# Kernel optimization log

Hardware: AMD Instinct MI355X
Metric: run time of the kernel (lower is better)

Reference implementation:

```python
import jax, jax.numpy as jnp
import numpy as np


def setup_inputs() -> dict:
    key = jax.random.key(0)
    k1, k2, k3, k4 = jax.random.split(key, 4)
    B, S, H = 1, 2048, 3072
    E, I = 4, 8192  # num_experts, intermediate_size
    x = jax.random.normal(k1, (B, S, H), dtype=jnp.float32)
    gate_w = jax.random.normal(k2, (E, H), dtype=jnp.float32) * 0.02
    w_gate_up = jax.random.normal(k3, (E, 2 * I, H), dtype=jnp.float32) * 0.02
    w_down = jax.random.normal(k4, (E, H, I), dtype=jnp.float32) * 0.02
    return {"x": x, "gate_w": gate_w, "w_gate_up": w_gate_up, "w_down": w_down, "top_k": 2}


def reference(x, gate_w, w_gate_up, w_down, top_k):
    # x: [B, S, H]; gate_w: [E, H]; w_gate_up: [E, 2I, H]; w_down: [E, H, I]
    B, S, H = x.shape
    E = gate_w.shape[0]
    # Gating: softmax over experts, then top-k values/indices
    logits = jnp.einsum('bsh,eh->bse', x, gate_w)
    probs = jax.nn.softmax(logits, axis=-1)
    gate_values, gate_indices = jax.lax.top_k(probs, top_k)  # [B, S, k]
    # Dense all-expert SwiGLU MLP (as in the original module)
    xf = x.reshape(-1, H)                                     # [N, H]
    up_states = jnp.einsum('nh,eih->nei', xf, w_gate_up)      # [N, E, 2I]
    gate, up = jnp.split(up_states, 2, axis=-1)               # [N, E, I] each
    hidden = up * jax.nn.silu(gate)                           # SwiGLU
    expert_out = jnp.einsum('nei,ehi->neh', hidden, w_down)   # [N, E, H]
    expert_out = expert_out.reshape(B, S, E, H)
    # Gather selected experts and combine with gate values
    sel = jnp.take_along_axis(expert_out, gate_indices[..., None], axis=2)  # [B, S, k, H]
    moe_output = jnp.sum(sel * gate_values[..., None], axis=2)              # [B, S, H]
    return moe_output
```

## Files before the change

kernel.cpp:

```cpp
#include <hip/hip_runtime.h>

#define S 2048
#define Hd 3072
#define NE 4
#define Id 8192
#define BK 64
#define RMAX 5120

typedef __attribute__((ext_vector_type(8))) short short8;
typedef __attribute__((ext_vector_type(4))) float f32x4;

__device__ __forceinline__ unsigned short f2bf(float f) {
    unsigned u = __builtin_bit_cast(unsigned, f);
    u += 0x7FFFu + ((u >> 16) & 1u);
    return (unsigned short)(u >> 16);
}

__device__ __forceinline__ void gload_lds16(const void* g, void* l) {
    __builtin_amdgcn_global_load_lds(
        (const __attribute__((address_space(1))) unsigned int*)g,
        (__attribute__((address_space(3))) unsigned int*)l,
        16, 0, 0);
}

#define BAR_SB()  { __builtin_amdgcn_s_barrier(); __builtin_amdgcn_sched_barrier(0); }
#define LGKM0_SB() { asm volatile("s_waitcnt lgkmcnt(0)" ::: "memory"); __builtin_amdgcn_sched_barrier(0); }
#define VM6_SB()  { asm volatile("s_waitcnt vmcnt(6)" ::: "memory"); __builtin_amdgcn_sched_barrier(0); }

__global__ void gate_topk_kernel(const float* __restrict__ x,
                                 const float* __restrict__ gw,
                                 int* __restrict__ tok_e,
                                 float* __restrict__ tok_v) {
    const int t = blockIdx.x;
    const int lane = threadIdx.x & 63;
    const int wave = threadIdx.x >> 6;
    __shared__ float logits[NE];
    const float* xp = x + (size_t)t * Hd;
    const float* wp = gw + (size_t)wave * Hd;
    float s = 0.f;
    for (int h = lane; h < Hd; h += 64) s += xp[h] * wp[h];
#pragma unroll
    for (int o = 32; o > 0; o >>= 1) s += __shfl_xor(s, o);
    if (lane == 0) logits[wave] = s;
    __syncthreads();
    if (threadIdx.x == 0) {
        float m = logits[0];
#pragma unroll
        for (int e = 1; e < NE; e++) m = fmaxf(m, logits[e]);
        float p[NE]; float sum = 0.f;
#pragma unroll
        for (int e = 0; e < NE; e++) { p[e] = expf(logits[e] - m); sum += p[e]; }
        float inv = 1.f / sum;
#pragma unroll
        for (int e = 0; e < NE; e++) p[e] *= inv;
        int e0 = 0; float v0 = p[0];
#pragma unroll
        for (int e = 1; e < NE; e++) if (p[e] > v0) { e0 = e; v0 = p[e]; }
        int e1 = -1; float v1 = -1.f;
#pragma unroll
        for (int e = 0; e < NE; e++) if (e != e0 && p[e] > v1) { e1 = e; v1 = p[e]; }
        tok_e[t * 2] = e0; tok_e[t * 2 + 1] = e1;
        tok_v[t * 2] = v0; tok_v[t * 2 + 1] = v1;
    }
}

__global__ void route_kernel(const int* __restrict__ tok_e, const float* __restrict__ tok_v,
                             int* __restrict__ row_token, float* __restrict__ row_gate,
                             int* __restrict__ offsets) {
    __shared__ int cnt[NE], cur[NE], offs[NE + 1];
    const int tid = threadIdx.x;
    if (tid < NE) { cnt[tid] = 0; cur[tid] = 0; }
    __syncthreads();
    for (int i = tid; i < S * 2; i += 256) atomicAdd(&cnt[tok_e[i]], 1);
    __syncthreads();
    if (tid == 0) {
        int o = 0;
        for (int e = 0; e < NE; e++) { offs[e] = o; o += (cnt[e] + 255) / 256 * 256; }
        offs[NE] = o;
        for (int e = 0; e <= NE; e++) offsets[e] = offs[e];
    }
    __syncthreads();
    for (int r = tid; r < RMAX; r += 256) { row_token[r] = 0; row_gate[r] = 0.f; }
    __syncthreads();
    for (int i = tid; i < S * 2; i += 256) {
        int e = tok_e[i];
        int pos = atomicAdd(&cur[e], 1);
        int r = offs[e] + pos;
        row_token[r] = i >> 1;
        row_gate[r] = tok_v[i];
    }
}

__global__ void cvt_bf16_kernel(const float* __restrict__ src,
                                unsigned short* __restrict__ dst, size_t n8) {
    size_t stride = (size_t)gridDim.x * blockDim.x;
    for (size_t i = (size_t)blockIdx.x * blockDim.x + threadIdx.x; i < n8; i += stride) {
        size_t b = i * 8;
        f32x4 a = *(const f32x4*)(src + b);
        f32x4 c = *(const f32x4*)(src + b + 4);
        union { unsigned short u[8]; short8 v; } o;
#pragma unroll
        for (int j = 0; j < 4; j++) { o.u[j] = f2bf(a[j]); o.u[4 + j] = f2bf(c[j]); }
        *(short8*)(dst + b) = o.v;
    }
}


#define ST_A0(buf, k) { gload_lds16(aP[0] + (k), &Ald[buf][raD[0]][0]); gload_lds16(aP[1] + (k), &Ald[buf][raD[1]][0]); }
#define ST_A1(buf, k) { gload_lds16(aP[2] + (k), &Ald[buf][raD[2]][0]); gload_lds16(aP[3] + (k), &Ald[buf][raD[3]][0]); }
#define ST_B0(buf, k) { gload_lds16(bP[0] + (k), &Bld[buf][rbD[0]][0]); gload_lds16(bP[1] + (k), &Bld[buf][rbD[1]][0]); }
#define ST_B1(buf, k) { gload_lds16(bP[2] + (k), &Bld[buf][rbD[2]][0]); gload_lds16(bP[3] + (k), &Bld[buf][rbD[3]][0]); }

#define READ_AFL(b) _Pragma("unroll") for (int mi = 0; mi < 4; mi++) _Pragma("unroll") for (int kk = 0; kk < 2; kk++) { \
    int row = wm * 128 + mi * 16 + c16; int slot = ((kk << 2) + c4) ^ l7; \
    afL[mi][kk] = *(const short8*)&Ald[b][row][slot * 8]; }
#define READ_AFH(b) _Pragma("unroll") for (int mi = 0; mi < 4; mi++) _Pragma("unroll") for (int kk = 0; kk < 2; kk++) { \
    int row = wm * 128 + 64 + mi * 16 + c16; int slot = ((kk << 2) + c4) ^ l7; \
    afH[mi][kk] = *(const short8*)&Ald[b][row][slot * 8]; }
#define READ_BFL(b) _Pragma("unroll") for (int n = 0; n < 2; n++) _Pragma("unroll") for (int kk = 0; kk < 2; kk++) { \
    int row = wn * 64 + n * 16 + c16; int slot = ((kk << 2) + c4) ^ l7; \
    bfL[n][kk] = *(const short8*)&Bld[b][row][slot * 8]; }
#define READ_BFH(b) _Pragma("unroll") for (int n = 0; n < 2; n++) _Pragma("unroll") for (int kk = 0; kk < 2; kk++) { \
    int row = wn * 64 + 32 + n * 16 + c16; int slot = ((kk << 2) + c4) ^ l7; \
    bfH[n][kk] = *(const short8*)&Bld[b][row][slot * 8]; }

#define MFMA_Q(AF, BF, MO, NO) _Pragma("unroll") for (int mi = 0; mi < 4; mi++) \
    _Pragma("unroll") for (int n = 0; n < 2; n++) _Pragma("unroll") for (int kk = 0; kk < 2; kk++) \
        acc[mi + MO][n + NO] = __builtin_amdgcn_mfma_f32_16x16x32_bf16(AF[mi][kk], BF[n][kk], acc[mi + MO][n + NO], 0, 0, 0);

#define KTILE_BODY(bR, bW, kN, kNN) { \
    short8 afL[4][2], afH[4][2], bfL[2][2], bfH[2][2]; \
    READ_AFL(bR); READ_BFL(bR); \
    ST_B1(bW, kN); \
    BAR_SB(); LGKM0_SB(); \
    __builtin_amdgcn_s_setprio(1); MFMA_Q(afL, bfL, 0, 0); __builtin_amdgcn_s_setprio(0); \
    BAR_SB(); \
    READ_AFH(bR); \
    ST_A0(bR, kNN); \
    BAR_SB(); LGKM0_SB(); \
    __builtin_amdgcn_s_setprio(1); MFMA_Q(afH, bfL, 4, 0); __builtin_amdgcn_s_setprio(0); \
    BAR_SB(); \
    READ_BFH(bR); \
    ST_B0(bR, kNN); \
    BAR_SB(); LGKM0_SB(); \
    __builtin_amdgcn_s_setprio(1); MFMA_Q(afL, bfH, 0, 2); __builtin_amdgcn_s_setprio(0); \
    BAR_SB(); \
    ST_A1(bR, kNN); \
    BAR_SB(); \
    __builtin_amdgcn_s_setprio(1); MFMA_Q(afH, bfH, 4, 2); __builtin_amdgcn_s_setprio(0); \
    VM6_SB(); BAR_SB(); }

__global__ __launch_bounds__(512, 2)
void gemm1_8p_kernel(const unsigned short* __restrict__ xb,
                     const unsigned short* __restrict__ wgu_b,
                     const int* __restrict__ row_token,
                     const int* __restrict__ offsets,
                     unsigned short* __restrict__ hidden) {
    __shared__ unsigned short Ald[2][256][BK];
    __shared__ unsigned short Bld[2][256][BK];

    const int rt = blockIdx.x, ct = blockIdx.y;
    const int rbase = rt * 256;
    if (rbase >= offsets[4]) return;
    int e = 3;
    if (rbase < offsets[1]) e = 0;
    else if (rbase < offsets[2]) e = 1;
    else if (rbase < offsets[3]) e = 2;

    const int tid = threadIdx.x;
    const int l = tid & 63;
    const int w = tid >> 6;
    const int wm = w >> 2, wn = w & 3;
    const int lr = l >> 3;
    const int g8 = ((l & 7) ^ lr) << 3;
    const int c16 = l & 15, c4 = l >> 4, l7 = l & 7;

    const unsigned short* aP[4]; int raD[4];
    const unsigned short* bP[4]; int rbD[4];
#pragma unroll
    for (int j = 0; j < 4; j++) {
        int r0 = w * 8 + (j & 1) * 128 + (j >> 1) * 64;
        raD[j] = r0;
        int tok = row_token[rbase + r0 + lr];
        aP[j] = xb + (size_t)tok * Hd + g8;
        int rb0 = (w & 3) * 8 + (w >> 2) * 64 + (j & 1) * 128 + (j >> 1) * 32;
        rbD[j] = rb0;
        int brow = rb0 + lr;
        int f = brow >> 4;
        size_t wr = (size_t)e * (2 * Id) + (size_t)(f & 1) * Id
                  + (size_t)ct * 128 + ((f >> 1) << 4) + (brow & 15);
        bP[j] = wgu_b + wr * Hd + g8;
    }

    f32x4 acc[8][4];
#pragma unroll
    for (int mi = 0; mi < 8; mi++)
#pragma unroll
        for (int n = 0; n < 4; n++) acc[mi][n] = (f32x4)0.f;

    ST_A0(0, 0); ST_B0(0, 0); ST_A1(0, 0); ST_B1(0, 0);
    ST_A0(1, BK); ST_B0(1, BK); ST_A1(1, BK);
    VM6_SB(); BAR_SB();

    const int nt = Hd / BK;
    for (int t = 0; t < nt; ++t) {
        const int bR = t & 1, bW = bR ^ 1;
        const int kN  = (t + 1 < nt ? t + 1 : nt - 1) * BK;
        const int kNN = (t + 2 < nt ? t + 2 : nt - 1) * BK;
        KTILE_BODY(bR, bW, kN, kNN);
    }
    asm volatile("s_waitcnt vmcnt(0)" ::: "memory");

#pragma unroll
    for (int mi = 0; mi < 8; mi++)
#pragma unroll
        for (int np = 0; np < 2; np++) {
            int col = ct * 128 + (wn * 2 + np) * 16 + c16;
#pragma unroll
            for (int q = 0; q < 4; q++) {
                int row = rbase + wm * 128 + mi * 16 + c4 * 4 + q;
                float gv = acc[mi][2 * np][q], uv = acc[mi][2 * np + 1][q];
                float h = uv * gv / (1.f + expf(-gv));
                hidden[(size_t)row * Id + col] = f2bf(h);
            }
        }
}

__global__ __launch_bounds__(512, 2)
void gemm2_8p_kernel(const unsigned short* __restrict__ hidden,
                     const unsigned short* __restrict__ wd_b,
                     const int* __restrict__ row_token,
                     const float* __restrict__ row_gate,
                     const int* __restrict__ offsets,
                     float* __restrict__ out) {
    __shared__ unsigned short Ald[2][256][BK];
    __shared__ unsigned short Bld[2][256][BK];

    const int rt = blockIdx.x, ct = blockIdx.y;
    const int rbase = rt * 256;
    if (rbase >= offsets[4]) return;
    int e = 3;
    if (rbase < offsets[1]) e = 0;
    else if (rbase < offsets[2]) e = 1;
    else if (rbase < offsets[3]) e = 2;

    const int tid = threadIdx.x;
    const int l = tid & 63;
    const int w = tid >> 6;
    const int wm = w >> 2, wn = w & 3;
    const int lr = l >> 3;
    const int g8 = ((l & 7) ^ lr) << 3;
    const int c16 = l & 15, c4 = l >> 4, l7 = l & 7;

    const unsigned short* aP[4]; int raD[4];
    const unsigned short* bP[4]; int rbD[4];
#pragma unroll
    for (int j = 0; j < 4; j++) {
        int r0 = w * 8 + (j & 1) * 128 + (j >> 1) * 64;
        raD[j] = r0;
        aP[j] = hidden + (size_t)(rbase + r0 + lr) * Id + g8;
        int rb0 = (w & 3) * 8 + (w >> 2) * 64 + (j & 1) * 128 + (j >> 1) * 32;
        rbD[j] = rb0;
        size_t wr = (size_t)e * Hd + (size_t)ct * 256 + rb0 + lr;
        bP[j] = wd_b + wr * Id + g8;
    }

    f32x4 acc[8][4];
#pragma unroll
    for (int mi = 0; mi < 8; mi++)
#pragma unroll
        for (int n = 0; n < 4; n++) acc[mi][n] = (f32x4)0.f;

    ST_A0(0, 0); ST_B0(0, 0); ST_A1(0, 0); ST_B1(0, 0);
    ST_A0(1, BK); ST_B0(1, BK); ST_A1(1, BK);
    VM6_SB(); BAR_SB();

    const int nt = Id / BK;
    for (int t = 0; t < nt; ++t) {
        const int bR = t & 1, bW = bR ^ 1;
        const int kN  = (t + 1 < nt ? t + 1 : nt - 1) * BK;
        const int kNN = (t + 2 < nt ? t + 2 : nt - 1) * BK;
        KTILE_BODY(bR, bW, kN, kNN);
    }
    asm volatile("s_waitcnt vmcnt(0)" ::: "memory");

#pragma unroll
    for (int mi = 0; mi < 8; mi++)
#pragma unroll
        for (int n = 0; n < 4; n++) {
            int col = ct * 256 + wn * 64 + n * 16 + c16;
#pragma unroll
            for (int q = 0; q < 4; q++) {
                int r = rbase + wm * 128 + mi * 16 + c4 * 4 + q;
                int tok = row_token[r];
                float gv = row_gate[r];
                if (gv != 0.f)
                    atomicAdd(&out[(size_t)tok * Hd + col], gv * acc[mi][n][q]);
            }
        }
}


__global__ __launch_bounds__(256, 2)
void gemm1_f32_kernel(const unsigned short* __restrict__ xb,
                      const float* __restrict__ wgu,
                      const int* __restrict__ row_token,
                      const int* __restrict__ offsets,
                      unsigned short* __restrict__ hidden) {
    __shared__ unsigned short As[128][BK];
    __shared__ unsigned short Bg[128][BK];
    __shared__ unsigned short Bu[128][BK];

    const int rt = blockIdx.x, ct = blockIdx.y;
    const int rbase = rt * 128;
    if (rbase >= offsets[4]) return;
    int e = 3;
    if (rbase < offsets[1]) e = 0;
    else if (rbase < offsets[2]) e = 1;
    else if (rbase < offsets[3]) e = 2;

    const int tid = threadIdx.x;
    const int lane = tid & 63;
    const int wave = tid >> 6;
    const int wm = wave >> 1, wn = wave & 1;

    const unsigned short* asrc[4];
#pragma unroll
    for (int i2 = 0; i2 < 4; i2++) {
        int sgi = i2 * 4 + wave;
        int row = sgi * 8 + (lane >> 3);
        int g = (lane & 7) ^ (row & 7);
        int tok = row_token[rbase + row];
        asrc[i2] = xb + (size_t)tok * Hd + g * 8;
    }
    const int col = tid >> 1;
    const int half = tid & 1;
    const size_t grow = (size_t)e * (2 * Id) + (size_t)ct * 128 + col;
    const float* bsrc_g = wgu + grow * Hd + half * 32;
    const float* bsrc_u = wgu + (grow + (size_t)Id) * Hd + half * 32;
    const int csw = col & 7;

    f32x4 accg[4][4], accu[4][4];
#pragma unroll
    for (int m = 0; m < 4; m++)
#pragma unroll
        for (int n = 0; n < 4; n++) { accg[m][n] = (f32x4)0.f; accu[m][n] = (f32x4)0.f; }

    for (int k0 = 0; k0 < Hd; k0 += BK) {
        __syncthreads();
#pragma unroll
        for (int i2 = 0; i2 < 4; i2++) {
            int sgi = i2 * 4 + wave;
            gload_lds16(asrc[i2] + k0, &As[sgi * 8][0]);
        }
        {
            const float* pg = bsrc_g + k0;
            const float* pu = bsrc_u + k0;
            f32x4 vg[8], vu[8];
#pragma unroll
            for (int j = 0; j < 8; j++) vg[j] = *(const f32x4*)(pg + j * 4);
#pragma unroll
            for (int j = 0; j < 8; j++) vu[j] = *(const f32x4*)(pu + j * 4);
#pragma unroll
            for (int j = 0; j < 4; j++) {
                union { unsigned short u[8]; short8 v8; } wg_, wu_;
#pragma unroll
                for (int q = 0; q < 4; q++) {
                    wg_.u[q] = f2bf(vg[2 * j][q]); wg_.u[4 + q] = f2bf(vg[2 * j + 1][q]);
                    wu_.u[q] = f2bf(vu[2 * j][q]); wu_.u[4 + q] = f2bf(vu[2 * j + 1][q]);
                }
                int gs = (half * 4 + j) ^ csw;
                *(short8*)&Bg[col][gs * 8] = wg_.v8;
                *(short8*)&Bu[col][gs * 8] = wu_.v8;
            }
        }
        __syncthreads();
#pragma unroll
        for (int kk = 0; kk < 2; kk++) {
            short8 af[4], bgf[4], buf_[4];
#pragma unroll
            for (int m = 0; m < 4; m++) {
                int r = wm * 64 + m * 16 + (lane & 15);
                int slot = (kk * 4 + (lane >> 4)) ^ (r & 7);
                af[m] = *(const short8*)&As[r][slot * 8];
            }
#pragma unroll
            for (int n = 0; n < 4; n++) {
                int c = wn * 64 + n * 16 + (lane & 15);
                int slot = (kk * 4 + (lane >> 4)) ^ (c & 7);
                bgf[n] = *(const short8*)&Bg[c][slot * 8];
                buf_[n] = *(const short8*)&Bu[c][slot * 8];
            }
#pragma unroll
            for (int m = 0; m < 4; m++)
#pragma unroll
                for (int n = 0; n < 4; n++) {
                    accg[m][n] = __builtin_amdgcn_mfma_f32_16x16x32_bf16(af[m], bgf[n], accg[m][n], 0, 0, 0);
                    accu[m][n] = __builtin_amdgcn_mfma_f32_16x16x32_bf16(af[m], buf_[n], accu[m][n], 0, 0, 0);
                }
        }
    }
#pragma unroll
    for (int m = 0; m < 4; m++) {
#pragma unroll
        for (int n = 0; n < 4; n++) {
            int c = ct * 128 + wn * 64 + n * 16 + (lane & 15);
#pragma unroll
            for (int q = 0; q < 4; q++) {
                int r = rbase + wm * 64 + m * 16 + (lane >> 4) * 4 + q;
                float g = accg[m][n][q], u = accu[m][n][q];
                float hval = u * g / (1.f + expf(-g));
                hidden[(size_t)r * Id + c] = f2bf(hval);
            }
        }
    }
}

__global__ __launch_bounds__(256, 2)
void gemm2_f32_kernel(const unsigned short* __restrict__ hidden,
                      const float* __restrict__ wd,
                      const int* __restrict__ row_token,
                      const float* __restrict__ row_gate,
                      const int* __restrict__ offsets,
                      float* __restrict__ out) {
    __shared__ unsigned short As[128][BK];
    __shared__ unsigned short Bs[128][BK];

    const int rt = blockIdx.x, ct = blockIdx.y;
    const int rbase = rt * 128;
    if (rbase >= offsets[4]) return;
    int e = 3;
    if (rbase < offsets[1]) e = 0;
    else if (rbase < offsets[2]) e = 1;
    else if (rbase < offsets[3]) e = 2;

    const int tid = threadIdx.x;
    const int lane = tid & 63;
    const int wave = tid >> 6;
    const int wm = wave >> 1, wn = wave & 1;

    const unsigned short* asrc[4];
#pragma unroll
    for (int i2 = 0; i2 < 4; i2++) {
        int sgi = i2 * 4 + wave;
        int row = sgi * 8 + (lane >> 3);
        int g = (lane & 7) ^ (row & 7);
        asrc[i2] = hidden + (size_t)(rbase + row) * Id + g * 8;
    }
    const int col = tid >> 1;
    const int half = tid & 1;
    const float* bsrc = wd + ((size_t)e * Hd + (size_t)ct * 128 + col) * Id + half * 32;
    const int csw = col & 7;

    f32x4 acc[4][4];
#pragma unroll
    for (int m = 0; m < 4; m++)
#pragma unroll
        for (int n = 0; n < 4; n++) acc[m][n] = (f32x4)0.f;

    for (int k0 = 0; k0 < Id; k0 += BK) {
        __syncthreads();
#pragma unroll
        for (int i2 = 0; i2 < 4; i2++) {
            int sgi = i2 * 4 + wave;
            gload_lds16(asrc[i2] + k0, &As[sgi * 8][0]);
        }
        {
            const float* pb = bsrc + k0;
            f32x4 vb[8];
#pragma unroll
            for (int j = 0; j < 8; j++) vb[j] = *(const f32x4*)(pb + j * 4);
#pragma unroll
            for (int j = 0; j < 4; j++) {
                union { unsigned short u[8]; short8 v8; } wb_;
#pragma unroll
                for (int q = 0; q < 4; q++) {
                    wb_.u[q] = f2bf(vb[2 * j][q]); wb_.u[4 + q] = f2bf(vb[2 * j + 1][q]);
                }
                int gs = (half * 4 + j) ^ csw;
                *(short8*)&Bs[col][gs * 8] = wb_.v8;
            }
        }
        __syncthreads();
#pragma unroll
        for (int kk = 0; kk < 2; kk++) {
            short8 af[4], bf[4];
#pragma unroll
            for (int m = 0; m < 4; m++) {
                int r = wm * 64 + m * 16 + (lane & 15);
                int slot = (kk * 4 + (lane >> 4)) ^ (r & 7);
                af[m] = *(const short8*)&As[r][slot * 8];
            }
#pragma unroll
            for (int n = 0; n < 4; n++) {
                int c = wn * 64 + n * 16 + (lane & 15);
                int slot = (kk * 4 + (lane >> 4)) ^ (c & 7);
                bf[n] = *(const short8*)&Bs[c][slot * 8];
            }
#pragma unroll
            for (int m = 0; m < 4; m++)
#pragma unroll
                for (int n = 0; n < 4; n++)
                    acc[m][n] = __builtin_amdgcn_mfma_f32_16x16x32_bf16(af[m], bf[n], acc[m][n], 0, 0, 0);
        }
    }
#pragma unroll
    for (int m = 0; m < 4; m++) {
#pragma unroll
        for (int n = 0; n < 4; n++) {
            int c = ct * 128 + wn * 64 + n * 16 + (lane & 15);
#pragma unroll
            for (int q = 0; q < 4; q++) {
                int r = rbase + wm * 64 + m * 16 + (lane >> 4) * 4 + q;
                int tok = row_token[r];
                float gv = row_gate[r];
                if (gv != 0.f)
                    atomicAdd(&out[(size_t)tok * Hd + c], gv * acc[m][n][q]);
            }
        }
    }
}

extern "C" void kernel_launch(void* const* d_in, const int* in_sizes, int n_in,
                              void* d_out, int out_size, void* d_ws, size_t ws_size,
                              hipStream_t stream) {
    const float* x   = (const float*)d_in[0];
    const float* gw  = (const float*)d_in[1];
    const float* wgu = (const float*)d_in[2];
    const float* wd  = (const float*)d_in[3];
    float* out = (float*)d_out;

    const size_t n_wgu = (size_t)NE * 2 * Id * Hd;
    const size_t n_wd  = (size_t)NE * Hd * Id;

    char* ws = (char*)d_ws;
    size_t o = 0;
    auto alloc = [&](size_t bytes) { void* p = ws + o; o = (o + bytes + 255) & ~(size_t)255; return p; };
    unsigned short* xb      = (unsigned short*)alloc((size_t)S * Hd * 2);
    unsigned short* hidden  = (unsigned short*)alloc((size_t)RMAX * Id * 2);
    int*   row_token = (int*)alloc(RMAX * 4);
    float* row_gate  = (float*)alloc(RMAX * 4);
    int*   offsets   = (int*)alloc(8 * 4);
    int*   tok_e     = (int*)alloc(S * 2 * 4);
    float* tok_v     = (float*)alloc(S * 2 * 4);
    unsigned short* wgu_b = (unsigned short*)alloc(n_wgu * 2);
    unsigned short* wd_b  = (unsigned short*)alloc(n_wd * 2);
    const bool big = (ws_size >= o);

    hipMemsetAsync(d_out, 0, (size_t)S * Hd * 4, stream);
    gate_topk_kernel<<<S, 256, 0, stream>>>(x, gw, tok_e, tok_v);
    route_kernel<<<1, 256, 0, stream>>>(tok_e, tok_v, row_token, row_gate, offsets);
    cvt_bf16_kernel<<<1024, 256, 0, stream>>>(x, xb, (size_t)S * Hd / 8);

    if (big) {
        cvt_bf16_kernel<<<2048, 256, 0, stream>>>(wgu, wgu_b, n_wgu / 8);
        cvt_bf16_kernel<<<2048, 256, 0, stream>>>(wd, wd_b, n_wd / 8);
        gemm1_8p_kernel<<<dim3(RMAX / 256, Id / 128), 512, 0, stream>>>(
            xb, wgu_b, row_token, offsets, hidden);
        gemm2_8p_kernel<<<dim3(RMAX / 256, Hd / 256), 512, 0, stream>>>(
            hidden, wd_b, row_token, row_gate, offsets, out);
    } else {
        gemm1_f32_kernel<<<dim3(RMAX / 128, Id / 128), 256, 0, stream>>>(
            xb, wgu, row_token, offsets, hidden);
        gemm2_f32_kernel<<<dim3(RMAX / 128, Hd / 128), 256, 0, stream>>>(
            hidden, wd, row_token, row_gate, offsets, out);
    }
}
```

Before: 1.238 ms.

## Remap GEMM blocks per XCD, shrink gemm2 N-tile, widen bf16 conversion

Both GEMMs now launch a 1D grid whose block index is remapped so that each XCD owns a contiguous range of column tiles. This is meant to improve L2 reuse of the weight tiles. gemm2 halves its N tile to 128 columns with fewer B loads and accumulators, which gives more blocks to fill the CUs at the cost of more re-reads of the A (hidden) tile. The conversion kernel now processes 16 floats per thread with more blocks. The sched_barrier after s_barrier is dropped, which gives the compiler more freedom to schedule but may disturb the hand-tuned ordering.

```diff
diff --git a/kernel.cpp b/kernel.cpp
--- a/kernel.cpp
+++ b/kernel.cpp
@@ -23,9 +23,10 @@
         16, 0, 0);
 }
 
-#define BAR_SB()  { __builtin_amdgcn_s_barrier(); __builtin_amdgcn_sched_barrier(0); }
+#define BAR() __builtin_amdgcn_s_barrier();
 #define LGKM0_SB() { asm volatile("s_waitcnt lgkmcnt(0)" ::: "memory"); __builtin_amdgcn_sched_barrier(0); }
 #define VM6_SB()  { asm volatile("s_waitcnt vmcnt(6)" ::: "memory"); __builtin_amdgcn_sched_barrier(0); }
+#define VM4_SB()  { asm volatile("s_waitcnt vmcnt(4)" ::: "memory"); __builtin_amdgcn_sched_barrier(0); }
 
 __global__ void gate_topk_kernel(const float* __restrict__ x,
                                  const float* __restrict__ gw,
@@ -92,16 +93,22 @@
 }
 
 __global__ void cvt_bf16_kernel(const float* __restrict__ src,
-                                unsigned short* __restrict__ dst, size_t n8) {
+                                unsigned short* __restrict__ dst, size_t n16) {
     size_t stride = (size_t)gridDim.x * blockDim.x;
-    for (size_t i = (size_t)blockIdx.x * blockDim.x + threadIdx.x; i < n8; i += stride) {
-        size_t b = i * 8;
-        f32x4 a = *(const f32x4*)(src + b);
-        f32x4 c = *(const f32x4*)(src + b + 4);
-        union { unsigned short u[8]; short8 v; } o;
-#pragma unroll
-        for (int j = 0; j < 4; j++) { o.u[j] = f2bf(a[j]); o.u[4 + j] = f2bf(c[j]); }
-        *(short8*)(dst + b) = o.v;
+    for (size_t i = (size_t)blockIdx.x * blockDim.x + threadIdx.x; i < n16; i += stride) {
+        size_t b = i * 16;
+        f32x4 a0 = *(const f32x4*)(src + b);
+        f32x4 a1 = *(const f32x4*)(src + b + 4);
+        f32x4 a2 = *(const f32x4*)(src + b + 8);
+        f32x4 a3 = *(const f32x4*)(src + b + 12);
+        union { unsigned short u[8]; short8 v; } o0, o1;
+#pragma unroll
+        for (int j = 0; j < 4; j++) {
+            o0.u[j] = f2bf(a0[j]); o0.u[4 + j] = f2bf(a1[j]);
+            o1.u[j] = f2bf(a2[j]); o1.u[4 + j] = f2bf(a3[j]);
+        }
+        *(short8*)(dst + b) = o0.v;
+        *(short8*)(dst + b + 8) = o1.v;
     }
 }
 
@@ -117,38 +124,6 @@
 #define READ_AFH(b) _Pragma("unroll") for (int mi = 0; mi < 4; mi++) _Pragma("unroll") for (int kk = 0; kk < 2; kk++) { \
     int row = wm * 128 + 64 + mi * 16 + c16; int slot = ((kk << 2) + c4) ^ l7; \
     afH[mi][kk] = *(const short8*)&Ald[b][row][slot * 8]; }
-#define READ_BFL(b) _Pragma("unroll") for (int n = 0; n < 2; n++) _Pragma("unroll") for (int kk = 0; kk < 2; kk++) { \
-    int row = wn * 64 + n * 16 + c16; int slot = ((kk << 2) + c4) ^ l7; \
-    bfL[n][kk] = *(const short8*)&Bld[b][row][slot * 8]; }
-#define READ_BFH(b) _Pragma("unroll") for (int n = 0; n < 2; n++) _Pragma("unroll") for (int kk = 0; kk < 2; kk++) { \
-    int row = wn * 64 + 32 + n * 16 + c16; int slot = ((kk << 2) + c4) ^ l7; \
-    bfH[n][kk] = *(const short8*)&Bld[b][row][slot * 8]; }
-
-#define MFMA_Q(AF, BF, MO, NO) _Pragma("unroll") for (int mi = 0; mi < 4; mi++) \
-    _Pragma("unroll") for (int n = 0; n < 2; n++) _Pragma("unroll") for (int kk = 0; kk < 2; kk++) \
-        acc[mi + MO][n + NO] = __builtin_amdgcn_mfma_f32_16x16x32_bf16(AF[mi][kk], BF[n][kk], acc[mi + MO][n + NO], 0, 0, 0);
-
-#define KTILE_BODY(bR, bW, kN, kNN) { \
-    short8 afL[4][2], afH[4][2], bfL[2][2], bfH[2][2]; \
-    READ_AFL(bR); READ_BFL(bR); \
-    ST_B1(bW, kN); \
-    BAR_SB(); LGKM0_SB(); \
-    __builtin_amdgcn_s_setprio(1); MFMA_Q(afL, bfL, 0, 0); __builtin_amdgcn_s_setprio(0); \
-    BAR_SB(); \
-    READ_AFH(bR); \
-    ST_A0(bR, kNN); \
-    BAR_SB(); LGKM0_SB(); \
-    __builtin_amdgcn_s_setprio(1); MFMA_Q(afH, bfL, 4, 0); __builtin_amdgcn_s_setprio(0); \
-    BAR_SB(); \
-    READ_BFH(bR); \
-    ST_B0(bR, kNN); \
-    BAR_SB(); LGKM0_SB(); \
-    __builtin_amdgcn_s_setprio(1); MFMA_Q(afL, bfH, 0, 2); __builtin_amdgcn_s_setprio(0); \
-    BAR_SB(); \
-    ST_A1(bR, kNN); \
-    BAR_SB(); \
-    __builtin_amdgcn_s_setprio(1); MFMA_Q(afH, bfH, 4, 2); __builtin_amdgcn_s_setprio(0); \
-    VM6_SB(); BAR_SB(); }
 
 __global__ __launch_bounds__(512, 2)
 void gemm1_8p_kernel(const unsigned short* __restrict__ xb,
@@ -159,7 +134,10 @@
     __shared__ unsigned short Ald[2][256][BK];
     __shared__ unsigned short Bld[2][256][BK];
 
-    const int rt = blockIdx.x, ct = blockIdx.y;
+    const int id = blockIdx.x;
+    const int xcd = id & 7, jj = id >> 3;
+    const int ct = xcd * 8 + jj / 20;
+    const int rt = jj % 20;
     const int rbase = rt * 256;
     if (rbase >= offsets[4]) return;
     int e = 3;
@@ -200,14 +178,80 @@
 
     ST_A0(0, 0); ST_B0(0, 0); ST_A1(0, 0); ST_B1(0, 0);
     ST_A0(1, BK); ST_B0(1, BK); ST_A1(1, BK);
-    VM6_SB(); BAR_SB();
+    VM6_SB(); BAR();
 
     const int nt = Hd / BK;
     for (int t = 0; t < nt; ++t) {
         const int bR = t & 1, bW = bR ^ 1;
         const int kN  = (t + 1 < nt ? t + 1 : nt - 1) * BK;
         const int kNN = (t + 2 < nt ? t + 2 : nt - 1) * BK;
-        KTILE_BODY(bR, bW, kN, kNN);
+        short8 afL[4][2], afH[4][2], bfL[2][2], bfH[2][2];
+        READ_AFL(bR);
+#pragma unroll
+        for (int n = 0; n < 2; n++)
+#pragma unroll
+            for (int kk = 0; kk < 2; kk++) {
+                int row = wn * 64 + n * 16 + c16;
+                int slot = ((kk << 2) + c4) ^ l7;
+                bfL[n][kk] = *(const short8*)&Bld[bR][row][slot * 8];
+            }
+        ST_B1(bW, kN);
+        BAR(); LGKM0_SB();
+        __builtin_amdgcn_s_setprio(1);
+#pragma unroll
+        for (int mi = 0; mi < 4; mi++)
+#pragma unroll
+            for (int n = 0; n < 2; n++)
+#pragma unroll
+                for (int kk = 0; kk < 2; kk++)
+                    acc[mi][n] = __builtin_amdgcn_mfma_f32_16x16x32_bf16(afL[mi][kk], bfL[n][kk], acc[mi][n], 0, 0, 0);
+        __builtin_amdgcn_s_setprio(0);
+        BAR();
+        READ_AFH(bR);
+        ST_A0(bR, kNN);
+        BAR(); LGKM0_SB();
+        __builtin_amdgcn_s_setprio(1);
+#pragma unroll
+        for (int mi = 0; mi < 4; mi++)
+#pragma unroll
+            for (int n = 0; n < 2; n++)
+#pragma unroll
+                for (int kk = 0; kk < 2; kk++)
+                    acc[mi + 4][n] = __builtin_amdgcn_mfma_f32_16x16x32_bf16(afH[mi][kk], bfL[n][kk], acc[mi + 4][n], 0, 0, 0);
+        __builtin_amdgcn_s_setprio(0);
+        BAR();
+#pragma unroll
+        for (int n = 0; n < 2; n++)
+#pragma unroll
+            for (int kk = 0; kk < 2; kk++) {
+                int row = wn * 64 + 32 + n * 16 + c16;
+                int slot = ((kk << 2) + c4) ^ l7;
+                bfH[n][kk] = *(const short8*)&Bld[bR][row][slot * 8];
+            }
+        ST_B0(bR, kNN);
+        BAR(); LGKM0_SB();
+        __builtin_amdgcn_s_setprio(1);
+#pragma unroll
+        for (int mi = 0; mi < 4; mi++)
+#pragma unroll
+            for (int n = 0; n < 2; n++)
+#pragma unroll
+                for (int kk = 0; kk < 2; kk++)
+                    acc[mi][n + 2] = __builtin_amdgcn_mfma_f32_16x16x32_bf16(afL[mi][kk], bfH[n][kk], acc[mi][n + 2], 0, 0, 0);
+        __builtin_amdgcn_s_setprio(0);
+        BAR();
+        ST_A1(bR, kNN);
+        BAR();
+        __builtin_amdgcn_s_setprio(1);
+#pragma unroll
+        for (int mi = 0; mi < 4; mi++)
+#pragma unroll
+            for (int n = 0; n < 2; n++)
+#pragma unroll
+                for (int kk = 0; kk < 2; kk++)
+                    acc[mi + 4][n + 2] = __builtin_amdgcn_mfma_f32_16x16x32_bf16(afH[mi][kk], bfH[n][kk], acc[mi + 4][n + 2], 0, 0, 0);
+        __builtin_amdgcn_s_setprio(0);
+        VM6_SB(); BAR();
     }
     asm volatile("s_waitcnt vmcnt(0)" ::: "memory");
 
@@ -234,9 +278,12 @@
                      const int* __restrict__ offsets,
                      float* __restrict__ out) {
     __shared__ unsigned short Ald[2][256][BK];
-    __shared__ unsigned short Bld[2][256][BK];
-
-    const int rt = blockIdx.x, ct = blockIdx.y;
+    __shared__ unsigned short Bld[2][128][BK];
+
+    const int id = blockIdx.x;
+    const int xcd = id & 7, jj = id >> 3;
+    const int ct = xcd * 3 + jj / 20;
+    const int rt = jj % 20;
     const int rbase = rt * 256;
     if (rbase >= offsets[4]) return;
     int e = 3;
@@ -253,42 +300,96 @@
     const int c16 = l & 15, c4 = l >> 4, l7 = l & 7;
 
     const unsigned short* aP[4]; int raD[4];
-    const unsigned short* bP[4]; int rbD[4];
+    const unsigned short* bP[2]; int rbD[2];
 #pragma unroll
     for (int j = 0; j < 4; j++) {
         int r0 = w * 8 + (j & 1) * 128 + (j >> 1) * 64;
         raD[j] = r0;
         aP[j] = hidden + (size_t)(rbase + r0 + lr) * Id + g8;
-        int rb0 = (w & 3) * 8 + (w >> 2) * 64 + (j & 1) * 128 + (j >> 1) * 32;
+    }
+#pragma unroll
+    for (int j = 0; j < 2; j++) {
+        int rb0 = w * 8 + j * 64;
         rbD[j] = rb0;
-        size_t wr = (size_t)e * Hd + (size_t)ct * 256 + rb0 + lr;
-        bP[j] = wd_b + wr * Id + g8;
-    }
-
-    f32x4 acc[8][4];
+        bP[j] = wd_b + ((size_t)e * Hd + (size_t)ct * 128 + rb0 + lr) * Id + g8;
+    }
+
+    f32x4 acc[8][2];
 #pragma unroll
     for (int mi = 0; mi < 8; mi++)
 #pragma unroll
-        for (int n = 0; n < 4; n++) acc[mi][n] = (f32x4)0.f;
-
-    ST_A0(0, 0); ST_B0(0, 0); ST_A1(0, 0); ST_B1(0, 0);
-    ST_A0(1, BK); ST_B0(1, BK); ST_A1(1, BK);
-    VM6_SB(); BAR_SB();
+        for (int n = 0; n < 2; n++) acc[mi][n] = (f32x4)0.f;
+
+    ST_A0(0, 0); ST_A1(0, 0); ST_B0(0, 0);
+    ST_A0(1, BK); ST_A1(1, BK);
+    VM4_SB(); BAR();
 
     const int nt = Id / BK;
     for (int t = 0; t < nt; ++t) {
         const int bR = t & 1, bW = bR ^ 1;
         const int kN  = (t + 1 < nt ? t + 1 : nt - 1) * BK;
         const int kNN = (t + 2 < nt ? t + 2 : nt - 1) * BK;
-        KTILE_BODY(bR, bW, kN, kNN);
+        short8 afL[4][2], afH[4][2], bf0[2], bf1[2];
+        READ_AFL(bR);
+#pragma unroll
+        for (int kk = 0; kk < 2; kk++) {
+            int row = wn * 32 + c16;
+            int slot = ((kk << 2) + c4) ^ l7;
+            bf0[kk] = *(const short8*)&Bld[bR][row][slot * 8];
+        }
+        ST_B0(bW, kN);
+        BAR(); LGKM0_SB();
+        __builtin_amdgcn_s_setprio(1);
+#pragma unroll
+        for (int mi = 0; mi < 4; mi++)
+#pragma unroll
+            for (int kk = 0; kk < 2; kk++)
+                acc[mi][0] = __builtin_amdgcn_mfma_f32_16x16x32_bf16(afL[mi][kk], bf0[kk], acc[mi][0], 0, 0, 0);
+        __builtin_amdgcn_s_setprio(0);
+        BAR();
+        READ_AFH(bR);
+        ST_A0(bR, kNN);
+        BAR(); LGKM0_SB();
+        __builtin_amdgcn_s_setprio(1);
+#pragma unroll
+        for (int mi = 0; mi < 4; mi++)
+#pragma unroll
+            for (int kk = 0; kk < 2; kk++)
+                acc[mi + 4][0] = __builtin_amdgcn_mfma_f32_16x16x32_bf16(afH[mi][kk], bf0[kk], acc[mi + 4][0], 0, 0, 0);
+        __builtin_amdgcn_s_setprio(0);
+        BAR();
+#pragma unroll
+        for (int kk = 0; kk < 2; kk++) {
+            int row = wn * 32 + 16 + c16;
+            int slot = ((kk << 2) + c4) ^ l7;
+            bf1[kk] = *(const short8*)&Bld[bR][row][slot * 8];
+        }
+        ST_A1(bR, kNN);
+        BAR(); LGKM0_SB();
+        __builtin_amdgcn_s_setprio(1);
+#pragma unroll
+        for (int mi = 0; mi < 4; mi++)
+#pragma unroll
+            for (int kk = 0; kk < 2; kk++)
+                acc[mi][1] = __builtin_amdgcn_mfma_f32_16x16x32_bf16(afL[mi][kk], bf1[kk], acc[mi][1], 0, 0, 0);
+        __builtin_amdgcn_s_setprio(0);
+        BAR();
+        __builtin_amdgcn_s_setprio(1);
+#pragma unroll
+        for (int mi = 0; mi < 4; mi++)
+#pragma unroll
+            for (int kk = 0; kk < 2; kk++)
+                acc[mi + 4][1] = __builtin_amdgcn_mfma_f32_16x16x32_bf16(afH[mi][kk], bf1[kk], acc[mi + 4][1], 0, 0, 0);
+        __builtin_amdgcn_s_setprio(0);
+        VM4_SB(); BAR();
     }
     asm volatile("s_waitcnt vmcnt(0)" ::: "memory");
 
 #pragma unroll
     for (int mi = 0; mi < 8; mi++)
 #pragma unroll
-        for (int n = 0; n < 4; n++) {
-            int col = ct * 256 + wn * 64 + n * 16 + c16;
+        for (int n = 0; n < 2; n++) {
+            int col = ct * 128 + wn * 32 + n * 16 + c16;
 #pragma unroll
             for (int q = 0; q < 4; q++) {
                 int r = rbase + wm * 128 + mi * 16 + c4 * 4 + q;
@@ -550,15 +651,13 @@
     hipMemsetAsync(d_out, 0, (size_t)S * Hd * 4, stream);
     gate_topk_kernel<<<S, 256, 0, stream>>>(x, gw, tok_e, tok_v);
     route_kernel<<<1, 256, 0, stream>>>(tok_e, tok_v, row_token, row_gate, offsets);
-    cvt_bf16_kernel<<<1024, 256, 0, stream>>>(x, xb, (size_t)S * Hd / 8);
+    cvt_bf16_kernel<<<1024, 256, 0, stream>>>(x, xb, (size_t)S * Hd / 16);
 
     if (big) {
-        cvt_bf16_kernel<<<2048, 256, 0, stream>>>(wgu, wgu_b, n_wgu / 8);
-        cvt_bf16_kernel<<<2048, 256, 0, stream>>>(wd, wd_b, n_wd / 8);
-        gemm1_8p_kernel<<<dim3(RMAX / 256, Id / 128), 512, 0, stream>>>(
-            xb, wgu_b, row_token, offsets, hidden);
-        gemm2_8p_kernel<<<dim3(RMAX / 256, Hd / 256), 512, 0, stream>>>(
-            hidden, wd_b, row_token, row_gate, offsets, out);
+        cvt_bf16_kernel<<<4096, 256, 0, stream>>>(wgu, wgu_b, n_wgu / 16);
+        cvt_bf16_kernel<<<4096, 256, 0, stream>>>(wd, wd_b, n_wd / 16);
+        gemm1_8p_kernel<<<1280, 512, 0, stream>>>(xb, wgu_b, row_token, offsets, hidden);
+        gemm2_8p_kernel<<<480, 512, 0, stream>>>(hidden, wd_b, row_token, row_gate, offsets, out);
     } else {
         gemm1_f32_kernel<<<dim3(RMAX / 128, Id / 128), 256, 0, stream>>>(
             xb, wgu, row_token, offsets, hidden);
```

Result: slower. 1.291 ms (+4.3%).

## Remap gemm1 blocks per XCD, widen bf16 conversion, relax sched barriers

Applied to the files above, without the earlier changes.

The gemm1 grid is flattened to 1D and remapped so that blocks landing on the same XCD share weight column tiles and sweep all row tiles, which should improve L2 reuse of the bf16 weights. The bf16 conversion kernel now handles 16 elements per thread with a doubled grid to make fewer, wider memory accesses. The sched_barrier after each s_barrier is dropped so the compiler can reorder instructions across barriers. That reordering risks breaking the hand-tuned interleaving of LDS reads, global loads and MFMAs.

```diff
diff --git a/kernel.cpp b/kernel.cpp
--- a/kernel.cpp
+++ b/kernel.cpp
@@ -23,7 +23,7 @@
         16, 0, 0);
 }
 
-#define BAR_SB()  { __builtin_amdgcn_s_barrier(); __builtin_amdgcn_sched_barrier(0); }
+#define BAR() __builtin_amdgcn_s_barrier();
 #define LGKM0_SB() { asm volatile("s_waitcnt lgkmcnt(0)" ::: "memory"); __builtin_amdgcn_sched_barrier(0); }
 #define VM6_SB()  { asm volatile("s_waitcnt vmcnt(6)" ::: "memory"); __builtin_amdgcn_sched_barrier(0); }
 
@@ -92,16 +92,22 @@
 }
 
 __global__ void cvt_bf16_kernel(const float* __restrict__ src,
-                                unsigned short* __restrict__ dst, size_t n8) {
+                                unsigned short* __restrict__ dst, size_t n16) {
     size_t stride = (size_t)gridDim.x * blockDim.x;
-    for (size_t i = (size_t)blockIdx.x * blockDim.x + threadIdx.x; i < n8; i += stride) {
-        size_t b = i * 8;
-        f32x4 a = *(const f32x4*)(src + b);
-        f32x4 c = *(const f32x4*)(src + b + 4);
-        union { unsigned short u[8]; short8 v; } o;
-#pragma unroll
-        for (int j = 0; j < 4; j++) { o.u[j] = f2bf(a[j]); o.u[4 + j] = f2bf(c[j]); }
-        *(short8*)(dst + b) = o.v;
+    for (size_t i = (size_t)blockIdx.x * blockDim.x + threadIdx.x; i < n16; i += stride) {
+        size_t b = i * 16;
+        f32x4 a0 = *(const f32x4*)(src + b);
+        f32x4 a1 = *(const f32x4*)(src + b + 4);
+        f32x4 a2 = *(const f32x4*)(src + b + 8);
+        f32x4 a3 = *(const f32x4*)(src + b + 12);
+        union { unsigned short u[8]; short8 v; } o0, o1;
+#pragma unroll
+        for (int j = 0; j < 4; j++) {
+            o0.u[j] = f2bf(a0[j]); o0.u[4 + j] = f2bf(a1[j]);
+            o1.u[j] = f2bf(a2[j]); o1.u[4 + j] = f2bf(a3[j]);
+        }
+        *(short8*)(dst + b) = o0.v;
+        *(short8*)(dst + b + 8) = o1.v;
     }
 }
 
@@ -130,25 +136,29 @@
 
 #define KTILE_BODY(bR, bW, kN, kNN) { \
     short8 afL[4][2], afH[4][2], bfL[2][2], bfH[2][2]; \
+     \
     READ_AFL(bR); READ_BFL(bR); \
     ST_B1(bW, kN); \
-    BAR_SB(); LGKM0_SB(); \
+    BAR(); LGKM0_SB(); \
     __builtin_amdgcn_s_setprio(1); MFMA_Q(afL, bfL, 0, 0); __builtin_amdgcn_s_setprio(0); \
-    BAR_SB(); \
+    BAR(); \
+     \
     READ_AFH(bR); \
     ST_A0(bR, kNN); \
-    BAR_SB(); LGKM0_SB(); \
+    BAR(); LGKM0_SB(); \
     __builtin_amdgcn_s_setprio(1); MFMA_Q(afH, bfL, 4, 0); __builtin_amdgcn_s_setprio(0); \
-    BAR_SB(); \
+    BAR(); \
+     \
     READ_BFH(bR); \
     ST_B0(bR, kNN); \
-    BAR_SB(); LGKM0_SB(); \
+    BAR(); LGKM0_SB(); \
     __builtin_amdgcn_s_setprio(1); MFMA_Q(afL, bfH, 0, 2); __builtin_amdgcn_s_setprio(0); \
-    BAR_SB(); \
+    BAR(); \
+     \
     ST_A1(bR, kNN); \
-    BAR_SB(); \
+    BAR(); \
     __builtin_amdgcn_s_setprio(1); MFMA_Q(afH, bfH, 4, 2); __builtin_amdgcn_s_setprio(0); \
-    VM6_SB(); BAR_SB(); }
+    VM6_SB(); BAR(); }
 
 __global__ __launch_bounds__(512, 2)
 void gemm1_8p_kernel(const unsigned short* __restrict__ xb,
@@ -159,7 +169,10 @@
     __shared__ unsigned short Ald[2][256][BK];
     __shared__ unsigned short Bld[2][256][BK];
 
-    const int rt = blockIdx.x, ct = blockIdx.y;
+    const int id = blockIdx.x;
+    const int xcd = id & 7, jj = id >> 3;
+    const int ct = xcd * 8 + jj / 20;
+    const int rt = jj % 20;
     const int rbase = rt * 256;
     if (rbase >= offsets[4]) return;
     int e = 3;
@@ -200,7 +213,7 @@
 
     ST_A0(0, 0); ST_B0(0, 0); ST_A1(0, 0); ST_B1(0, 0);
     ST_A0(1, BK); ST_B0(1, BK); ST_A1(1, BK);
-    VM6_SB(); BAR_SB();
+    VM6_SB(); BAR();
 
     const int nt = Hd / BK;
     for (int t = 0; t < nt; ++t) {
@@ -273,7 +286,7 @@
 
     ST_A0(0, 0); ST_B0(0, 0); ST_A1(0, 0); ST_B1(0, 0);
     ST_A0(1, BK); ST_B0(1, BK); ST_A1(1, BK);
-    VM6_SB(); BAR_SB();
+    VM6_SB(); BAR();
 
     const int nt = Id / BK;
     for (int t = 0; t < nt; ++t) {
@@ -550,13 +563,12 @@
     hipMemsetAsync(d_out, 0, (size_t)S * Hd * 4, stream);
     gate_topk_kernel<<<S, 256, 0, stream>>>(x, gw, tok_e, tok_v);
     route_kernel<<<1, 256, 0, stream>>>(tok_e, tok_v, row_token, row_gate, offsets);
-    cvt_bf16_kernel<<<1024, 256, 0, stream>>>(x, xb, (size_t)S * Hd / 8);
+    cvt_bf16_kernel<<<1024, 256, 0, stream>>>(x, xb, (size_t)S * Hd / 16);
 
     if (big) {
-        cvt_bf16_kernel<<<2048, 256, 0, stream>>>(wgu, wgu_b, n_wgu / 8);
-        cvt_bf16_kernel<<<2048, 256, 0, stream>>>(wd, wd_b, n_wd / 8);
-        gemm1_8p_kernel<<<dim3(RMAX / 256, Id / 128), 512, 0, stream>>>(
-            xb, wgu_b, row_token, offsets, hidden);
+        cvt_bf16_kernel<<<4096, 256, 0, stream>>>(wgu, wgu_b, n_wgu / 16);
+        cvt_bf16_kernel<<<4096, 256, 0, stream>>>(wd, wd_b, n_wd / 16);
+        gemm1_8p_kernel<<<1280, 512, 0, stream>>>(xb, wgu_b, row_token, offsets, hidden);
         gemm2_8p_kernel<<<dim3(RMAX / 256, Hd / 256), 512, 0, stream>>>(
             hidden, wd_b, row_token, row_gate, offsets, out);
     } else {
```

Result: faster. 1.196 ms (-3.4%).
